# Kernel tuning notes

Measured on AMD Instinct MI355X. Metric: run time of the kernel, lower is better.

## Reference

```python
import jax, jax.numpy as jnp
import numpy as np

EPS_BN = 1e-5
CLAMP_MAX = 1e-10  # nn.Hardtanh(min_val=0, max_val=1e-10) on squared dists


def _three_nn(xyz1, xyz2):
    # xyz1: (b, n, 3), xyz2: (b, m, 3) -> sq dists (b, n, 3), idx (b, n, 3)
    d2 = (jnp.sum(xyz1 ** 2, -1, keepdims=True)
          - 2.0 * jnp.einsum('bnc,bmc->bnm', xyz1, xyz2)
          + jnp.sum(xyz2 ** 2, -1)[:, None, :])  # (b, n, m)
    neg, idx = jax.lax.top_k(-d2, 3)
    return -neg, idx


def _conv_bn_relu(x, W, b, g, beta):
    # x: (b, n, cin); 1x1 Conv2d == pointwise linear, BN over (batch, spatial)
    y = jnp.einsum('bnc,oc->bno', x, W) + b
    mean = jnp.mean(y, axis=(0, 1))
    var = jnp.mean((y - mean) ** 2, axis=(0, 1))
    y = (y - mean) * jax.lax.rsqrt(var + EPS_BN) * g + beta
    return jax.nn.relu(y)


def setup_inputs() -> dict:
    key = jax.random.key(0)
    ks = jax.random.split(key, 8)
    b, n, m, c1, c2 = 16, 4096, 1024, 256, 512
    mlp, dimin = [256, 256], [c1 + c2, 256]
    inp = {
        'xyz1': jax.random.normal(ks[0], (b, n, 3), jnp.float32),
        'xyz2': jax.random.normal(ks[1], (b, m, 3), jnp.float32),
        'points1': jax.random.normal(ks[2], (b, n, c1), jnp.float32),
        'points2': jax.random.normal(ks[3], (b, m, c2), jnp.float32),
        'W1': jax.random.normal(ks[4], (mlp[0], dimin[0]), jnp.float32) * 0.02,
        'b1': jnp.zeros((mlp[0],), jnp.float32),
        'g1': jnp.ones((mlp[0],), jnp.float32),
        'beta1': jnp.zeros((mlp[0],), jnp.float32),
        'W2': jax.random.normal(ks[5], (mlp[1], dimin[1]), jnp.float32) * 0.02,
        'b2': jnp.zeros((mlp[1],), jnp.float32),
        'g2': jnp.ones((mlp[1],), jnp.float32),
        'beta2': jnp.zeros((mlp[1],), jnp.float32),
    }
    return inp


def reference(xyz1, xyz2, points1, points2, W1, b1, g1, beta1, W2, b2, g2, beta2):
    dist, idx = _three_nn(xyz1, xyz2)                     # (b, n, 3)
    dist = jnp.clip(dist, 0.0, CLAMP_MAX)                 # Hardtanh(0, 1e-10)
    inv = 1.0 / dist
    weight = inv / jnp.sum(inv, axis=2, keepdims=True)    # (b, n, 3)
    neigh = jax.vmap(lambda p, i: p[i])(points2, idx)     # (b, n, 3, c2)
    interp = jnp.einsum('bnk,bnkc->bnc', weight, neigh)   # (b, n, c2)
    feat = jnp.concatenate([interp, points1], axis=2)     # (b, n, c2+c1)
    feat = _conv_bn_relu(feat, W1, b1, g1, beta1)
    feat = _conv_bn_relu(feat, W2, b2, g2, beta2)
    return jnp.transpose(feat, (0, 2, 1))                 # (b, c_out, n)
```

## Files before the change

kernel.cpp:

```cpp
#include <hip/hip_runtime.h>

typedef unsigned short u16;
typedef short sh8 __attribute__((ext_vector_type(8)));
typedef float floatx4 __attribute__((ext_vector_type(4)));
typedef float float4v __attribute__((ext_vector_type(4)));
typedef u16 us8 __attribute__((ext_vector_type(8)));
typedef u16 us4 __attribute__((ext_vector_type(4)));

#define NB    16
#define NPTS  4096
#define MPTS  1024
#define CC1   256
#define CC2   512
#define KK1   768
#define CCO   256
#define MT    (NB*NPTS)
#define MZ    (NB*MPTS)

__device__ __forceinline__ float b2f(u16 u) {
    union { unsigned i; float f; } v; v.i = ((unsigned)u) << 16; return v.f;
}
__device__ __forceinline__ u16 f2b(float f) {
    union { float f; unsigned i; } v; v.f = f;
    unsigned u = v.i;
    unsigned r = (u + 0x7fffu + ((u >> 16) & 1u)) >> 16;
    return (u16)r;
}
__device__ __forceinline__ float ldv(const void* p, size_t i, int f32) {
    return f32 ? ((const float*)p)[i] : b2f(((const u16*)p)[i]);
}
__device__ __forceinline__ void stv(void* p, size_t i, int f32, float v) {
    if (f32) ((float*)p)[i] = v; else ((u16*)p)[i] = f2b(v);
}
__device__ __forceinline__ void gl_lds16(const void* g, void* l) {
    __builtin_amdgcn_global_load_lds(
        (const __attribute__((address_space(1))) void*)g,
        (__attribute__((address_space(3))) void*)l, 16, 0, 0);
}

__global__ void Pointnet_fp_module_33071248179394_kernel(
        const unsigned* g1bits, int* flag, float* stats) {
    int i = blockIdx.x * 256 + threadIdx.x;
    stats[i] = 0.f;
    if (i == 0) flag[0] = (g1bits[0] == 0x3F800000u) ? 1 : 0;
}

__global__ __launch_bounds__(512) void three_nn_k(
        const int* flagp, const void* xyz1, const void* xyz2,
        int* nidx, float* nw) {
    __shared__ float4 P[MPTS];
    __shared__ float md[512][3];
    __shared__ int   mi[512][3];
    const int f32 = flagp[0];
    const int bi = blockIdx.x >> 6;
    const int chunk = blockIdx.x & 63;
    const int t = threadIdx.x;
    const int ql = t & 63, sp = t >> 6;

    for (int p = t; p < MPTS; p += 512) {
        size_t s = (size_t)(bi * MPTS + p) * 3;
        P[p] = make_float4(ldv(xyz2, s, f32), ldv(xyz2, s + 1, f32),
                           ldv(xyz2, s + 2, f32), 0.f);
    }
    __syncthreads();

    const int q = chunk * 64 + ql;
    size_t s1 = (size_t)(bi * NPTS + q) * 3;
    const float qx = ldv(xyz1, s1 + 0, f32);
    const float qy = ldv(xyz1, s1 + 1, f32);
    const float qz = ldv(xyz1, s1 + 2, f32);

    float d0 = 3e38f, d1 = 3e38f, dv2 = 3e38f;
    int i0 = -1, i1 = -1, i2 = -1;
    const int jbeg = sp * 128, jend = jbeg + 128;
    #pragma unroll 4
    for (int j = jbeg; j < jend; j++) {
        float4 p = P[j];
        float dx = qx - p.x;
        float dy = qy - p.y;
        float dz = qz - p.z;
        float dd = fmaf(dx, dx, fmaf(dy, dy, dz * dz));
        if (dd < dv2) {
            if (dd < d0)      { dv2 = d1; i2 = i1; d1 = d0; i1 = i0; d0 = dd; i0 = j; }
            else if (dd < d1) { dv2 = d1; i2 = i1; d1 = dd; i1 = j; }
            else              { dv2 = dd; i2 = j; }
        }
    }
    md[t][0] = d0;  md[t][1] = d1;  md[t][2] = dv2;
    mi[t][0] = i0;  mi[t][1] = i1;  mi[t][2] = i2;
    __syncthreads();

    if (t < 64) {
        float b0 = 3e38f, b1 = 3e38f, b2v = 3e38f;
        int j0 = -1, j1 = -1, j2 = -1;
        #pragma unroll
        for (int s = 0; s < 8; s++) {
            int base = s * 64 + t;
            #pragma unroll
            for (int k = 0; k < 3; k++) {
                float d = md[base][k];
                int ji = mi[base][k];
                if (d < b0)      { b2v = b1; j2 = j1; b1 = b0; j1 = j0; b0 = d; j0 = ji; }
                else if (d < b1) { b2v = b1; j2 = j1; b1 = d; j1 = ji; }
                else if (d < b2v){ b2v = d; j2 = ji; }
            }
        }
        float e0 = fminf(fmaxf(b0, 0.f), 1e-10f);
        float e1 = fminf(fmaxf(b1, 0.f), 1e-10f);
        float e2 = fminf(fmaxf(b2v, 0.f), 1e-10f);
        float v0 = 1.0f / e0, v1 = 1.0f / e1, v2 = 1.0f / e2;
        float s = v0 + v1 + v2;
        const size_t gq = ((size_t)bi * NPTS + chunk * 64 + t) * 3;
        nidx[gq + 0] = j0; nidx[gq + 1] = j1; nidx[gq + 2] = j2;
        nw[gq + 0] = v0 / s; nw[gq + 1] = v1 / s; nw[gq + 2] = v2 / s;
    }
}

__global__ __launch_bounds__(256) void cvt_w_k(
        const int* flagp, const void* W1, const void* W2,
        u16* Wa, u16* Wbp, u16* W2b) {
    const int f32 = flagp[0];
    const int i = blockIdx.x * 256 + threadIdx.x;
    if (i < CCO * CC2) {
        int r = i >> 9, c = i & 511;
        Wa[i] = f2b(ldv(W1, (size_t)r * KK1 + c, f32));
    } else if (i < CCO * CC2 + CCO * CC1) {
        int k = i - CCO * CC2;
        int r = k >> 8, c = k & 255;
        Wbp[k] = f2b(ldv(W1, (size_t)r * KK1 + CC2 + c, f32));
    } else {
        int k = i - CCO * CC2 - CCO * CC1;
        W2b[k] = f2b(ldv(W2, k, f32));
    }
}

__global__ __launch_bounds__(256) void cvt_pts_k(
        const int* flagp, const void* p2, const void* p1,
        u16* p2b, u16* p1b) {
    const int f32 = flagp[0];
    size_t i = ((size_t)blockIdx.x * 256 + threadIdx.x) * 8;
    const size_t N2 = (size_t)MZ * CC2;
    const void* src; u16* dst; size_t off;
    if (i < N2) { src = p2; dst = p2b; off = i; }
    else        { src = p1; dst = p1b; off = i - N2; }
    us8 o;
    if (f32) {
        float4v a = *(const float4v*)((const float*)src + off);
        float4v b = *(const float4v*)((const float*)src + off + 4);
        #pragma unroll
        for (int k = 0; k < 4; k++) { o[k] = f2b(a[k]); o[k + 4] = f2b(b[k]); }
    } else {
        o = *(const us8*)((const u16*)src + off);
    }
    *(us8*)(dst + off) = o;
}

template<int K, int NW>
__global__ __launch_bounds__(128 * NW, 2) void gemm_z_k(
        const int* flagp, const u16* __restrict__ A, const u16* __restrict__ B,
        u16* __restrict__ Y) {
    constexpr int T  = 128 * NW;
    constexpr int NT = NW * 64;
    __shared__ u16 As[128 * 32];
    __shared__ u16 Bs[NT * 32];
    const int tid = threadIdx.x;
    const int m0 = blockIdx.x * 128;
    const int n0 = blockIdx.y * NT;
    const int wave = tid >> 6, lane = tid & 63;
    const int wm = wave & 1, wn = wave >> 1;
    const int l16 = lane & 15, quad = lane >> 4;

    floatx4 acc[4][4];
    #pragma unroll
    for (int i = 0; i < 4; i++)
        #pragma unroll
        for (int j = 0; j < 4; j++)
            acc[i][j] = (floatx4){0.f, 0.f, 0.f, 0.f};

    for (int kb = 0; kb < K; kb += 32) {
        __syncthreads();
        #pragma unroll
        for (int c = tid; c < 512; c += T) {
            int row = c >> 2, c4 = c & 3;
            gl_lds16(A + (size_t)(m0 + row) * K + kb + c4 * 8, As + c * 8);
        }
        #pragma unroll
        for (int c = tid; c < NT * 4; c += T) {
            int row = c >> 2, c4 = c & 3;
            gl_lds16(B + (size_t)(n0 + row) * K + kb + c4 * 8, Bs + c * 8);
        }
        __syncthreads();

        sh8 af[4], bfr[4];
        #pragma unroll
        for (int i = 0; i < 4; i++)
            af[i] = *(const sh8*)(As + (wm * 64 + i * 16 + l16) * 32 + quad * 8);
        #pragma unroll
        for (int j = 0; j < 4; j++)
            bfr[j] = *(const sh8*)(Bs + (wn * 64 + j * 16 + l16) * 32 + quad * 8);
        #pragma unroll
        for (int i = 0; i < 4; i++)
            #pragma unroll
            for (int j = 0; j < 4; j++)
                acc[i][j] = __builtin_amdgcn_mfma_f32_16x16x32_bf16(
                                bfr[j], af[i], acc[i][j], 0, 0, 0);
    }

    #pragma unroll
    for (int i = 0; i < 4; i++) {
        int row = m0 + wm * 64 + i * 16 + l16;
        #pragma unroll
        for (int j = 0; j < 4; j++) {
            int colb = wn * 64 + j * 16 + quad * 4;
            us4 o;
            #pragma unroll
            for (int r = 0; r < 4; r++)
                o[r] = f2b(acc[i][j][r]);
            *(us4*)(Y + (size_t)row * CCO + n0 + colb) = o;
        }
    }
}

template<bool GATHER, bool BN1>
__global__ __launch_bounds__(512, 4) void gemm_mt_k(
        const int* flagp, const u16* __restrict__ A, const u16* __restrict__ B,
        const void* __restrict__ bias, const int* __restrict__ nidx,
        const float* __restrict__ nw, const u16* __restrict__ Z,
        u16* __restrict__ Y, float* __restrict__ sum, float* __restrict__ sq,
        const float* __restrict__ nsum, const float* __restrict__ nsq,
        const void* __restrict__ ng, const void* __restrict__ nbeta) {
    __shared__ u16 As[128 * 256];
    __shared__ float sSum[256], sSq[256];
    __shared__ int   sIdx[GATHER ? 384 : 1];
    __shared__ float sW[GATHER ? 384 : 1];
    __shared__ float ssc[BN1 ? 256 : 1], ssh[BN1 ? 256 : 1];
    const int f32 = flagp[0];
    const int tid = threadIdx.x;
    const int m0 = blockIdx.x * 128;
    const int wave = tid >> 6, lane = tid & 63;
    const int wm = wave & 1, wn = wave >> 1;
    const int l16 = lane & 15, quad = lane >> 4;

    if (tid < 256) {
        sSum[tid] = 0.f; sSq[tid] = 0.f;
        if (BN1) {
            const float invM = 1.0f / (float)MT;
            float mean = nsum[tid] * invM;
            float var = nsq[tid] * invM - mean * mean;
            float sc = rsqrtf(var + 1e-5f) * ldv(ng, tid, f32);
            ssc[tid] = sc;
            ssh[tid] = ldv(nbeta, tid, f32) - mean * sc;
        }
    }
    if (GATHER && tid < 128) {
        size_t q3 = (size_t)(m0 + tid) * 3;
        #pragma unroll
        for (int k = 0; k < 3; k++) {
            sIdx[tid * 3 + k] = nidx[q3 + k];
            sW[tid * 3 + k]   = nw[q3 + k];
        }
    }
    if (BN1) __syncthreads();

    #pragma unroll
    for (int c = tid; c < 4096; c += 512) {
        int r = c >> 5, cp = c & 31;
        int col = ((cp ^ (r & 7)) << 3);
        if (BN1) {
            us8 a = *(const us8*)(A + (size_t)(m0 + r) * 256 + col);
            us8 o;
            #pragma unroll
            for (int k = 0; k < 8; k++) {
                int ch = col + k;
                o[k] = f2b(fmaxf(b2f((u16)a[k]) * ssc[ch] + ssh[ch], 0.f));
            }
            *(us8*)(As + c * 8) = o;
        } else {
            gl_lds16(A + (size_t)(m0 + r) * 256 + col, As + c * 8);
        }
    }
    __syncthreads();

    floatx4 acc[4][4];
    #pragma unroll
    for (int i = 0; i < 4; i++)
        #pragma unroll
        for (int j = 0; j < 4; j++)
            acc[i][j] = (floatx4){0.f, 0.f, 0.f, 0.f};

    #pragma unroll 2
    for (int kb = 0; kb < 256; kb += 32) {
        sh8 af[4], bfr[4];
        #pragma unroll
        for (int j = 0; j < 4; j++)
            bfr[j] = *(const sh8*)(B + (size_t)(wn * 64 + j * 16 + l16) * 256
                                     + kb + quad * 8);
        #pragma unroll
        for (int i = 0; i < 4; i++) {
            int r = wm * 64 + i * 16 + l16;
            int cp = ((kb >> 3) + quad) ^ (l16 & 7);
            af[i] = *(const sh8*)(As + r * 256 + (cp << 3));
        }
        #pragma unroll
        for (int i = 0; i < 4; i++)
            #pragma unroll
            for (int j = 0; j < 4; j++)
                acc[i][j] = __builtin_amdgcn_mfma_f32_16x16x32_bf16(
                                bfr[j], af[i], acc[i][j], 0, 0, 0);
    }

    float bvv[4][4];
    #pragma unroll
    for (int j = 0; j < 4; j++)
        #pragma unroll
        for (int r = 0; r < 4; r++)
            bvv[j][r] = ldv(bias, wn * 64 + j * 16 + quad * 4 + r, f32);

    float cs[4][4], css[4][4];
    #pragma unroll
    for (int j = 0; j < 4; j++)
        #pragma unroll
        for (int r = 0; r < 4; r++) { cs[j][r] = 0.f; css[j][r] = 0.f; }

    const int zbase = GATHER ? ((m0 >> 12) << 10) : 0;
    #pragma unroll
    for (int i = 0; i < 4; i++) {
        int rl = wm * 64 + i * 16 + l16;
        const u16 *z0 = nullptr, *z1 = nullptr, *z2 = nullptr;
        float w0 = 0.f, w1 = 0.f, w2 = 0.f;
        if (GATHER) {
            int i0 = sIdx[rl * 3 + 0], i1 = sIdx[rl * 3 + 1], i2 = sIdx[rl * 3 + 2];
            w0 = sW[rl * 3 + 0]; w1 = sW[rl * 3 + 1]; w2 = sW[rl * 3 + 2];
            z0 = Z + (size_t)(zbase + i0) * CCO;
            z1 = Z + (size_t)(zbase + i1) * CCO;
            z2 = Z + (size_t)(zbase + i2) * CCO;
        }
        u16* yrow = Y + (size_t)(m0 + rl) * CCO;
        #pragma unroll
        for (int j = 0; j < 4; j++) {
            int colb = wn * 64 + j * 16 + quad * 4;
            us4 o;
            if (GATHER) {
                us4 zv0 = *(const us4*)(z0 + colb);
                us4 zv1 = *(const us4*)(z1 + colb);
                us4 zv2 = *(const us4*)(z2 + colb);
                #pragma unroll
                for (int r = 0; r < 4; r++) {
                    float v = acc[i][j][r] + bvv[j][r]
                            + w0 * b2f((u16)zv0[r]) + w1 * b2f((u16)zv1[r])
                            + w2 * b2f((u16)zv2[r]);
                    cs[j][r] += v; css[j][r] += v * v;
                    o[r] = f2b(v);
                }
            } else {
                #pragma unroll
                for (int r = 0; r < 4; r++) {
                    float v = acc[i][j][r] + bvv[j][r];
                    cs[j][r] += v; css[j][r] += v * v;
                    o[r] = f2b(v);
                }
            }
            *(us4*)(yrow + colb) = o;
        }
    }
    #pragma unroll
    for (int j = 0; j < 4; j++)
        #pragma unroll
        for (int r = 0; r < 4; r++) {
            float a = cs[j][r], b = css[j][r];
            #pragma unroll
            for (int m = 1; m < 16; m <<= 1) {
                a += __shfl_xor(a, m, 64);
                b += __shfl_xor(b, m, 64);
            }
            if (l16 == 0) {
                int cl = wn * 64 + j * 16 + quad * 4 + r;
                atomicAdd(&sSum[cl], a);
                atomicAdd(&sSq[cl], b);
            }
        }
    __syncthreads();
    if (tid < 256) {
        atomicAdd(&sum[tid], sSum[tid]);
        atomicAdd(&sq[tid], sSq[tid]);
    }
}

__global__ void bn_out_k(const int* flagp, const u16* Y, void* Out,
                         const float* sum, const float* sq,
                         const void* g, const void* beta) {
    __shared__ float tile[64][65];
    const int f32 = flagp[0];
    const int bi = blockIdx.z;
    const int p0 = blockIdx.x * 64;
    const int c0 = blockIdx.y * 64;
    const int t = threadIdx.x;
    const int cr = t & 63, rq = t >> 6;
    const float invM = 1.0f / (float)MT;

    const int c = c0 + cr;
    float mean = sum[c] * invM;
    float var = sq[c] * invM - mean * mean;
    float sc = rsqrtf(var + 1e-5f) * ldv(g, c, f32);
    float sh = ldv(beta, c, f32) - mean * sc;

    for (int r = rq; r < 64; r += 4) {
        int m = bi * NPTS + p0 + r;
        float v = b2f(Y[(size_t)m * CCO + c]) * sc + sh;
        tile[r][cr] = fmaxf(v, 0.f);
    }
    __syncthreads();
    for (int r = rq; r < 64; r += 4) {
        size_t o = ((size_t)bi * CCO + (c0 + r)) * NPTS + p0 + cr;
        stv(Out, o, f32, tile[cr][r]);
    }
}

extern "C" void kernel_launch(void* const* d_in, const int* in_sizes, int n_in,
                              void* d_out, int out_size, void* d_ws, size_t ws_size,
                              hipStream_t stream) {
    const void* xyz1    = d_in[0];
    const void* xyz2    = d_in[1];
    const void* points1 = d_in[2];
    const void* points2 = d_in[3];
    const void* W1      = d_in[4];
    const void* b1      = d_in[5];
    const void* g1      = d_in[6];
    const void* be1     = d_in[7];
    const void* W2      = d_in[8];
    const void* b2      = d_in[9];
    const void* g2      = d_in[10];
    const void* be2     = d_in[11];
    char* ws = (char*)d_ws;

    int*   flag  = (int*)(ws + 0);
    float* sum1  = (float*)(ws + 4096);
    float* sq1   = (float*)(ws + 5120);
    float* sum2  = (float*)(ws + 6144);
    float* sq2   = (float*)(ws + 7168);
    int*   nidx  = (int*)(ws + 20480);
    float* nw    = (float*)(ws + 806912);
    u16* Wa   = (u16*)(ws + 2097152);
    u16* Wbp  = (u16*)(ws + 2359296);
    u16* W2b  = (u16*)(ws + 2490368);
    u16* Z    = (u16*)(ws + 2621440);
    u16* p2b  = (u16*)(ws + 11010048ULL);
    u16* p1b  = (u16*)(ws + 27787264ULL);
    u16* y1   = (u16*)(ws + 61341696ULL);
    u16* y2   = (u16*)(ws + 94896128ULL);

    Pointnet_fp_module_33071248179394_kernel<<<dim3(16), dim3(256), 0, stream>>>(
        (const unsigned*)g1, flag, (float*)(ws + 4096));
    cvt_w_k<<<dim3(1024), dim3(256), 0, stream>>>(
        flag, W1, W2, Wa, Wbp, W2b);
    cvt_pts_k<<<dim3((MZ * CC2 + MT * CC1) / 2048), dim3(256), 0, stream>>>(
        flag, points2, points1, p2b, p1b);
    three_nn_k<<<dim3(1024), dim3(512), 0, stream>>>(flag, xyz1, xyz2, nidx, nw);
    gemm_z_k<CC2, 2><<<dim3(MZ / 128, 2), dim3(256), 0, stream>>>(
        flag, p2b, Wa, Z);
    gemm_mt_k<true, false><<<dim3(MT / 128), dim3(512), 0, stream>>>(
        flag, p1b, Wbp, b1, nidx, nw, Z, y1, sum1, sq1,
        nullptr, nullptr, nullptr, nullptr);
    gemm_mt_k<false, true><<<dim3(MT / 128), dim3(512), 0, stream>>>(
        flag, y1, W2b, b2, nullptr, nullptr, nullptr, y2, sum2, sq2,
        sum1, sq1, g1, be1);
    bn_out_k<<<dim3(64, 4, NB), dim3(256), 0, stream>>>(
        flag, y2, d_out, sum2, sq2, g2, be2);
}
```

Before: 331.2 us.

## Stage GEMM epilogue through LDS for coalesced gather, store and BN stats

The GEMM epilogue now writes fp32 accumulators into shared memory using a swizzled layout, in two halves of 64 rows. Threads then re-read them so each thread owns four consecutive channels of a row. The 3-NN gather from Z, the bf16 store of Y and the BN sum/sumsq accumulation therefore use wide, contiguous row accesses, and the per-channel shuffle reductions are replaced by one shared atomic per channel per thread. The cost is extra barriers and LDS round trips, plus reuse of the A-tile buffer as scratch.

Result: no change. 333.2 us (+0.6%).

```diff
diff --git a/kernel.cpp b/kernel.cpp
--- a/kernel.cpp
+++ b/kernel.cpp
@@ -316,69 +316,63 @@
         for (int r = 0; r < 4; r++)
             bvv[j][r] = ldv(bias, wn * 64 + j * 16 + quad * 4 + r, f32);
 
-    float cs[4][4], css[4][4];
-    #pragma unroll
-    for (int j = 0; j < 4; j++)
-        #pragma unroll
-        for (int r = 0; r < 4; r++) { cs[j][r] = 0.f; css[j][r] = 0.f; }
-
+    float* LF = (float*)As;
     const int zbase = GATHER ? ((m0 >> 12) << 10) : 0;
-    #pragma unroll
-    for (int i = 0; i < 4; i++) {
-        int rl = wm * 64 + i * 16 + l16;
-        const u16 *z0 = nullptr, *z1 = nullptr, *z2 = nullptr;
-        float w0 = 0.f, w1 = 0.f, w2 = 0.f;
-        if (GATHER) {
-            int i0 = sIdx[rl * 3 + 0], i1 = sIdx[rl * 3 + 1], i2 = sIdx[rl * 3 + 2];
-            w0 = sW[rl * 3 + 0]; w1 = sW[rl * 3 + 1]; w2 = sW[rl * 3 + 2];
-            z0 = Z + (size_t)(zbase + i0) * CCO;
-            z1 = Z + (size_t)(zbase + i1) * CCO;
-            z2 = Z + (size_t)(zbase + i2) * CCO;
-        }
-        u16* yrow = Y + (size_t)(m0 + rl) * CCO;
-        #pragma unroll
-        for (int j = 0; j < 4; j++) {
-            int colb = wn * 64 + j * 16 + quad * 4;
-            us4 o;
-            if (GATHER) {
-                us4 zv0 = *(const us4*)(z0 + colb);
-                us4 zv1 = *(const us4*)(z1 + colb);
-                us4 zv2 = *(const us4*)(z2 + colb);
+    const int ch_t = tid & 63;
+    float cs[4] = {0.f, 0.f, 0.f, 0.f}, css[4] = {0.f, 0.f, 0.f, 0.f};
+
+    #pragma unroll
+    for (int h = 0; h < 2; h++) {
+        __syncthreads();
+        if (wm == h) {
+            #pragma unroll
+            for (int i = 0; i < 4; i++) {
+                int rl = i * 16 + l16;
                 #pragma unroll
-                for (int r = 0; r < 4; r++) {
-                    float v = acc[i][j][r] + bvv[j][r]
-                            + w0 * b2f((u16)zv0[r]) + w1 * b2f((u16)zv1[r])
-                            + w2 * b2f((u16)zv2[r]);
-                    cs[j][r] += v; css[j][r] += v * v;
-                    o[r] = f2b(v);
-                }
-            } else {
-                #pragma unroll
-                for (int r = 0; r < 4; r++) {
-                    float v = acc[i][j][r] + bvv[j][r];
-                    cs[j][r] += v; css[j][r] += v * v;
-                    o[r] = f2b(v);
+                for (int j = 0; j < 4; j++) {
+                    int chs = (wn * 16 + j * 4 + quad) ^ (rl & 15);
+                    floatx4 v;
+                    #pragma unroll
+                    for (int r = 0; r < 4; r++)
+                        v[r] = acc[i][j][r] + bvv[j][r];
+                    *(floatx4*)(LF + rl * 256 + chs * 4) = v;
                 }
             }
-            *(us4*)(yrow + colb) = o;
-        }
-    }
-    #pragma unroll
-    for (int j = 0; j < 4; j++)
-        #pragma unroll
-        for (int r = 0; r < 4; r++) {
-            float a = cs[j][r], b = css[j][r];
-            #pragma unroll
-            for (int m = 1; m < 16; m <<= 1) {
-                a += __shfl_xor(a, m, 64);
-                b += __shfl_xor(b, m, 64);
+        }
+        __syncthreads();
+        #pragma unroll
+        for (int c = tid; c < 4096; c += 512) {
+            int rl = c >> 6;
+            int row = h * 64 + rl;
+            int chs = ch_t ^ (rl & 15);
+            floatx4 v = *(const floatx4*)(LF + rl * 256 + chs * 4);
+            if (GATHER) {
+                int i0 = sIdx[row * 3 + 0], i1 = sIdx[row * 3 + 1],
+                    i2 = sIdx[row * 3 + 2];
+                float w0 = sW[row * 3 + 0], w1 = sW[row * 3 + 1],
+                      w2 = sW[row * 3 + 2];
+                us4 zv0 = *(const us4*)(Z + (size_t)(zbase + i0) * CCO + ch_t * 4);
+                us4 zv1 = *(const us4*)(Z + (size_t)(zbase + i1) * CCO + ch_t * 4);
+                us4 zv2 = *(const us4*)(Z + (size_t)(zbase + i2) * CCO + ch_t * 4);
+                #pragma unroll
+                for (int r = 0; r < 4; r++)
+                    v[r] += w0 * b2f((u16)zv0[r]) + w1 * b2f((u16)zv1[r])
+                          + w2 * b2f((u16)zv2[r]);
             }
-            if (l16 == 0) {
-                int cl = wn * 64 + j * 16 + quad * 4 + r;
-                atomicAdd(&sSum[cl], a);
-                atomicAdd(&sSq[cl], b);
+            us4 o;
+            #pragma unroll
+            for (int r = 0; r < 4; r++) {
+                cs[r] += v[r]; css[r] += v[r] * v[r];
+                o[r] = f2b(v[r]);
             }
-        }
+            *(us4*)(Y + (size_t)(m0 + row) * CCO + ch_t * 4) = o;
+        }
+    }
+    #pragma unroll
+    for (int r = 0; r < 4; r++) {
+        atomicAdd(&sSum[ch_t * 4 + r], cs[r]);
+        atomicAdd(&sSq[ch_t * 4 + r], css[r]);
+    }
     __syncthreads();
     if (tid < 256) {
         atomicAdd(&sum[tid], sSum[tid]);
```

## Fuse fp32-to-bf16 input conversion into GEMM loads and shrink GEMM tiles

Applied to the files above, without the earlier changes.

Drops the separate points conversion kernel: both GEMMs now read the fp32 point features directly and convert to bf16 while filling shared memory, which saves one full write and re-read of the converted arrays. The weight conversion is merged into the init kernel, removing a launch. gemm_mt_k moves from 128-row, 512-thread tiles to 64-row, 256-thread tiles, halving LDS per block so more blocks fit per CU and the grid doubles. For fp32 inputs the A loads become synchronous register loads instead of direct-to-LDS loads, and the B weight tiles are reloaded twice as often in total.

Result: no change. 335.6 us (+1.3%).

```diff
diff --git a/kernel.cpp b/kernel.cpp
--- a/kernel.cpp
+++ b/kernel.cpp
@@ -38,11 +38,26 @@
         (__attribute__((address_space(3))) void*)l, 16, 0, 0);
 }
 
-__global__ void Pointnet_fp_module_33071248179394_kernel(
-        const unsigned* g1bits, int* flag, float* stats) {
-    int i = blockIdx.x * 256 + threadIdx.x;
-    stats[i] = 0.f;
-    if (i == 0) flag[0] = (g1bits[0] == 0x3F800000u) ? 1 : 0;
+__global__ __launch_bounds__(256) void Pointnet_fp_module_33071248179394_kernel(
+        const unsigned* g1bits, int* flag, float* stats,
+        const void* W1, const void* W2, u16* Wa, u16* Wbp, u16* W2b) {
+    const int f32 = (g1bits[0] == 0x3F800000u) ? 1 : 0;
+    const int i = blockIdx.x * 256 + threadIdx.x;
+    if (blockIdx.x == 0) {
+        for (int k = threadIdx.x; k < 1024; k += 256) stats[k] = 0.f;
+        if (threadIdx.x == 0) flag[0] = f32;
+    }
+    if (i < CCO * CC2) {
+        int r = i >> 9, c = i & 511;
+        Wa[i] = f2b(ldv(W1, (size_t)r * KK1 + c, f32));
+    } else if (i < CCO * CC2 + CCO * CC1) {
+        int k = i - CCO * CC2;
+        int r = k >> 8, c = k & 255;
+        Wbp[k] = f2b(ldv(W1, (size_t)r * KK1 + CC2 + c, f32));
+    } else {
+        int k = i - CCO * CC2 - CCO * CC1;
+        W2b[k] = f2b(ldv(W2, k, f32));
+    }
 }
 
 __global__ __launch_bounds__(512) void three_nn_k(
@@ -116,53 +131,15 @@
     }
 }
 
-__global__ __launch_bounds__(256) void cvt_w_k(
-        const int* flagp, const void* W1, const void* W2,
-        u16* Wa, u16* Wbp, u16* W2b) {
-    const int f32 = flagp[0];
-    const int i = blockIdx.x * 256 + threadIdx.x;
-    if (i < CCO * CC2) {
-        int r = i >> 9, c = i & 511;
-        Wa[i] = f2b(ldv(W1, (size_t)r * KK1 + c, f32));
-    } else if (i < CCO * CC2 + CCO * CC1) {
-        int k = i - CCO * CC2;
-        int r = k >> 8, c = k & 255;
-        Wbp[k] = f2b(ldv(W1, (size_t)r * KK1 + CC2 + c, f32));
-    } else {
-        int k = i - CCO * CC2 - CCO * CC1;
-        W2b[k] = f2b(ldv(W2, k, f32));
-    }
-}
-
-__global__ __launch_bounds__(256) void cvt_pts_k(
-        const int* flagp, const void* p2, const void* p1,
-        u16* p2b, u16* p1b) {
-    const int f32 = flagp[0];
-    size_t i = ((size_t)blockIdx.x * 256 + threadIdx.x) * 8;
-    const size_t N2 = (size_t)MZ * CC2;
-    const void* src; u16* dst; size_t off;
-    if (i < N2) { src = p2; dst = p2b; off = i; }
-    else        { src = p1; dst = p1b; off = i - N2; }
-    us8 o;
-    if (f32) {
-        float4v a = *(const float4v*)((const float*)src + off);
-        float4v b = *(const float4v*)((const float*)src + off + 4);
-        #pragma unroll
-        for (int k = 0; k < 4; k++) { o[k] = f2b(a[k]); o[k + 4] = f2b(b[k]); }
-    } else {
-        o = *(const us8*)((const u16*)src + off);
-    }
-    *(us8*)(dst + off) = o;
-}
-
 template<int K, int NW>
 __global__ __launch_bounds__(128 * NW, 2) void gemm_z_k(
-        const int* flagp, const u16* __restrict__ A, const u16* __restrict__ B,
+        const int* flagp, const void* __restrict__ A, const u16* __restrict__ B,
         u16* __restrict__ Y) {
     constexpr int T  = 128 * NW;
     constexpr int NT = NW * 64;
     __shared__ u16 As[128 * 32];
     __shared__ u16 Bs[NT * 32];
+    const int f32 = flagp[0];
     const int tid = threadIdx.x;
     const int m0 = blockIdx.x * 128;
     const int n0 = blockIdx.y * NT;
@@ -182,7 +159,18 @@
         #pragma unroll
         for (int c = tid; c < 512; c += T) {
             int row = c >> 2, c4 = c & 3;
-            gl_lds16(A + (size_t)(m0 + row) * K + kb + c4 * 8, As + c * 8);
+            if (f32) {
+                const float* ap = (const float*)A + (size_t)(m0 + row) * K + kb + c4 * 8;
+                float4v a = *(const float4v*)ap;
+                float4v b = *(const float4v*)(ap + 4);
+                us8 o;
+                #pragma unroll
+                for (int k = 0; k < 4; k++) { o[k] = f2b(a[k]); o[k + 4] = f2b(b[k]); }
+                *(us8*)(As + c * 8) = o;
+            } else {
+                gl_lds16((const u16*)A + (size_t)(m0 + row) * K + kb + c4 * 8,
+                         As + c * 8);
+            }
         }
         #pragma unroll
         for (int c = tid; c < NT * 4; c += T) {
@@ -222,37 +210,35 @@
 }
 
 template<bool GATHER, bool BN1>
-__global__ __launch_bounds__(512, 4) void gemm_mt_k(
-        const int* flagp, const u16* __restrict__ A, const u16* __restrict__ B,
-        const void* __restrict__ bias, const int* __restrict__ nidx,
-        const float* __restrict__ nw, const u16* __restrict__ Z,
+__global__ __launch_bounds__(256, 4) void gemm_mt_k(
+        const int* flagp, const void* __restrict__ Asrc,
+        const u16* __restrict__ B, const void* __restrict__ bias,
+        const int* __restrict__ nidx, const float* __restrict__ nw,
+        const u16* __restrict__ Zb,
         u16* __restrict__ Y, float* __restrict__ sum, float* __restrict__ sq,
         const float* __restrict__ nsum, const float* __restrict__ nsq,
         const void* __restrict__ ng, const void* __restrict__ nbeta) {
-    __shared__ u16 As[128 * 256];
+    __shared__ u16 As[64 * 256];
     __shared__ float sSum[256], sSq[256];
-    __shared__ int   sIdx[GATHER ? 384 : 1];
-    __shared__ float sW[GATHER ? 384 : 1];
+    __shared__ int   sIdx[GATHER ? 192 : 1];
+    __shared__ float sW[GATHER ? 192 : 1];
     __shared__ float ssc[BN1 ? 256 : 1], ssh[BN1 ? 256 : 1];
     const int f32 = flagp[0];
     const int tid = threadIdx.x;
-    const int m0 = blockIdx.x * 128;
-    const int wave = tid >> 6, lane = tid & 63;
-    const int wm = wave & 1, wn = wave >> 1;
+    const int m0 = blockIdx.x * 64;
+    const int wn = tid >> 6, lane = tid & 63;
     const int l16 = lane & 15, quad = lane >> 4;
 
-    if (tid < 256) {
-        sSum[tid] = 0.f; sSq[tid] = 0.f;
-        if (BN1) {
-            const float invM = 1.0f / (float)MT;
-            float mean = nsum[tid] * invM;
-            float var = nsq[tid] * invM - mean * mean;
-            float sc = rsqrtf(var + 1e-5f) * ldv(ng, tid, f32);
-            ssc[tid] = sc;
-            ssh[tid] = ldv(nbeta, tid, f32) - mean * sc;
-        }
-    }
-    if (GATHER && tid < 128) {
+    sSum[tid] = 0.f; sSq[tid] = 0.f;
+    if (BN1) {
+        const float invM = 1.0f / (float)MT;
+        float mean = nsum[tid] * invM;
+        float var = nsq[tid] * invM - mean * mean;
+        float sc = rsqrtf(var + 1e-5f) * ldv(ng, tid, f32);
+        ssc[tid] = sc;
+        ssh[tid] = ldv(nbeta, tid, f32) - mean * sc;
+    }
+    if (GATHER && tid < 64) {
         size_t q3 = (size_t)(m0 + tid) * 3;
         #pragma unroll
         for (int k = 0; k < 3; k++) {
@@ -263,20 +249,26 @@
     if (BN1) __syncthreads();
 
     #pragma unroll
-    for (int c = tid; c < 4096; c += 512) {
+    for (int c = tid; c < 2048; c += 256) {
         int r = c >> 5, cp = c & 31;
         int col = ((cp ^ (r & 7)) << 3);
         if (BN1) {
-            us8 a = *(const us8*)(A + (size_t)(m0 + r) * 256 + col);
+            us8 a = *(const us8*)((const u16*)Asrc + (size_t)(m0 + r) * 256 + col);
             us8 o;
             #pragma unroll
-            for (int k = 0; k < 8; k++) {
-                int ch = col + k;
-                o[k] = f2b(fmaxf(b2f((u16)a[k]) * ssc[ch] + ssh[ch], 0.f));
-            }
+            for (int k = 0; k < 8; k++)
+                o[k] = f2b(fmaxf(b2f((u16)a[k]) * ssc[col + k] + ssh[col + k], 0.f));
+            *(us8*)(As + c * 8) = o;
+        } else if (f32) {
+            const float* ap = (const float*)Asrc + (size_t)(m0 + r) * 256 + col;
+            float4v a = *(const float4v*)ap;
+            float4v b = *(const float4v*)(ap + 4);
+            us8 o;
+            #pragma unroll
+            for (int k = 0; k < 4; k++) { o[k] = f2b(a[k]); o[k + 4] = f2b(b[k]); }
             *(us8*)(As + c * 8) = o;
         } else {
-            gl_lds16(A + (size_t)(m0 + r) * 256 + col, As + c * 8);
+            gl_lds16((const u16*)Asrc + (size_t)(m0 + r) * 256 + col, As + c * 8);
         }
     }
     __syncthreads();
@@ -297,7 +289,7 @@
                                      + kb + quad * 8);
         #pragma unroll
         for (int i = 0; i < 4; i++) {
-            int r = wm * 64 + i * 16 + l16;
+            int r = i * 16 + l16;
             int cp = ((kb >> 3) + quad) ^ (l16 & 7);
             af[i] = *(const sh8*)(As + r * 256 + (cp << 3));
         }
@@ -325,15 +317,15 @@
     const int zbase = GATHER ? ((m0 >> 12) << 10) : 0;
     #pragma unroll
     for (int i = 0; i < 4; i++) {
-        int rl = wm * 64 + i * 16 + l16;
+        int rl = i * 16 + l16;
         const u16 *z0 = nullptr, *z1 = nullptr, *z2 = nullptr;
         float w0 = 0.f, w1 = 0.f, w2 = 0.f;
         if (GATHER) {
             int i0 = sIdx[rl * 3 + 0], i1 = sIdx[rl * 3 + 1], i2 = sIdx[rl * 3 + 2];
             w0 = sW[rl * 3 + 0]; w1 = sW[rl * 3 + 1]; w2 = sW[rl * 3 + 2];
-            z0 = Z + (size_t)(zbase + i0) * CCO;
-            z1 = Z + (size_t)(zbase + i1) * CCO;
-            z2 = Z + (size_t)(zbase + i2) * CCO;
+            z0 = Zb + (size_t)(zbase + i0) * CCO;
+            z1 = Zb + (size_t)(zbase + i1) * CCO;
+            z2 = Zb + (size_t)(zbase + i2) * CCO;
         }
         u16* yrow = Y + (size_t)(m0 + rl) * CCO;
         #pragma unroll
@@ -380,10 +372,8 @@
             }
         }
     __syncthreads();
-    if (tid < 256) {
-        atomicAdd(&sum[tid], sSum[tid]);
-        atomicAdd(&sq[tid], sSq[tid]);
-    }
+    atomicAdd(&sum[tid], sSum[tid]);
+    atomicAdd(&sq[tid], sSq[tid]);
 }
 
 __global__ void bn_out_k(const int* flagp, const u16* Y, void* Out,
@@ -444,24 +434,18 @@
     u16* Wbp  = (u16*)(ws + 2359296);
     u16* W2b  = (u16*)(ws + 2490368);
     u16* Z    = (u16*)(ws + 2621440);
-    u16* p2b  = (u16*)(ws + 11010048ULL);
-    u16* p1b  = (u16*)(ws + 27787264ULL);
-    u16* y1   = (u16*)(ws + 61341696ULL);
-    u16* y2   = (u16*)(ws + 94896128ULL);
-
-    Pointnet_fp_module_33071248179394_kernel<<<dim3(16), dim3(256), 0, stream>>>(
-        (const unsigned*)g1, flag, (float*)(ws + 4096));
-    cvt_w_k<<<dim3(1024), dim3(256), 0, stream>>>(
-        flag, W1, W2, Wa, Wbp, W2b);
-    cvt_pts_k<<<dim3((MZ * CC2 + MT * CC1) / 2048), dim3(256), 0, stream>>>(
-        flag, points2, points1, p2b, p1b);
+    u16* y1   = (u16*)(ws + 11010048ULL);
+    u16* y2   = (u16*)(ws + 44564480ULL);
+
+    Pointnet_fp_module_33071248179394_kernel<<<dim3(1024), dim3(256), 0, stream>>>(
+        (const unsigned*)g1, flag, (float*)(ws + 4096), W1, W2, Wa, Wbp, W2b);
     three_nn_k<<<dim3(1024), dim3(512), 0, stream>>>(flag, xyz1, xyz2, nidx, nw);
     gemm_z_k<CC2, 2><<<dim3(MZ / 128, 2), dim3(256), 0, stream>>>(
-        flag, p2b, Wa, Z);
-    gemm_mt_k<true, false><<<dim3(MT / 128), dim3(512), 0, stream>>>(
-        flag, p1b, Wbp, b1, nidx, nw, Z, y1, sum1, sq1,
+        flag, points2, Wa, Z);
+    gemm_mt_k<true, false><<<dim3(MT / 64), dim3(256), 0, stream>>>(
+        flag, points1, Wbp, b1, nidx, nw, Z, y1, sum1, sq1,
         nullptr, nullptr, nullptr, nullptr);
-    gemm_mt_k<false, true><<<dim3(MT / 128), dim3(512), 0, stream>>>(
+    gemm_mt_k<false, true><<<dim3(MT / 64), dim3(256), 0, stream>>>(
         flag, y1, W2b, b2, nullptr, nullptr, nullptr, y2, sum2, sq2,
         sum1, sq1, g1, be1);
     bn_out_k<<<dim3(64, 4, NB), dim3(256), 0, stream>>>(
```
